# Kernel tuning notes

Hardware: AMD Instinct MI355X
Metric: run time of the kernel (lower is better)

The kernel has to match this reference:

```python
import jax, jax.numpy as jnp
import numpy as np

B, N, IN_DIM, OUT_DIM, H = 8, 1024, 512, 512, 8
SUP = OUT_DIM // H  # support_dim per head = 64


def setup_inputs() -> dict:
    key = jax.random.key(0)
    ks = jax.random.split(key, 6)
    # 0/1 dense adjacency with self-loops so no row is fully masked
    A = jax.random.randint(ks[0], (B, N, N), 0, 2).astype(jnp.float32)
    A = jnp.maximum(A, jnp.eye(N, dtype=jnp.float32)[None])
    X = jax.random.normal(ks[1], (B, N, IN_DIM), dtype=jnp.float32)
    # parameters, uniform(-1/sqrt(fan_last), 1/sqrt(fan_last)) as in reset_parameters
    sw = 1.0 / np.sqrt(SUP)
    W = jax.random.uniform(ks[2], (H, IN_DIM, SUP), minval=-sw, maxval=sw, dtype=jnp.float32)
    w1 = jax.random.uniform(ks[3], (H, SUP), minval=-sw, maxval=sw, dtype=jnp.float32)
    w2 = jax.random.uniform(ks[4], (H, SUP), minval=-sw, maxval=sw, dtype=jnp.float32)
    b = jax.random.uniform(ks[5], (2, H), minval=-1.0, maxval=1.0, dtype=jnp.float32)
    b1, b2 = b[0], b[1]
    return {"A": A, "X": X, "W": W, "w1": w1, "b1": b1, "w2": w2, "b2": b2}


def reference(A, X, W, w1, b1, w2, b2):
    # per-head projection: [B,H,N,SUP]
    inputs = jnp.einsum('bni,hio->bhno', X, W)
    # additive attention logits: self_fc [B,H,N,1] + neigh_fc [B,H,1,N]
    self_fc = jnp.einsum('bhno,ho->bhn', inputs, w1) + b1[None, :, None]
    neigh_fc = jnp.einsum('bhno,ho->bhn', inputs, w2) + b2[None, :, None]
    logits = jax.nn.leaky_relu(self_fc[..., :, None] + neigh_fc[..., None, :], 0.01)
    mask = -1e9 * (1.0 - A)  # [B,N,N]
    alphas = jax.nn.softmax(logits + mask[:, None], axis=-1)  # [B,H,N,N]
    out = jnp.einsum('bhnm,bhmo->bhno', alphas, inputs)
    out = jax.nn.relu(out)  # default activation = torch.relu
    # concat heads on last dim (head i contiguous), matching torch.cat
    return out.transpose(0, 2, 1, 3).reshape(B, N, H * SUP)
```

## Files before the change

kernel.cpp:

```cpp
#include <hip/hip_runtime.h>
#include <hip/hip_fp16.h>

#define BB 8
#define NN 1024
#define IN_DIM 512
#define HH 8
#define SUP 64
#define HS (HH * SUP)

typedef _Float16 half8 __attribute__((ext_vector_type(8)));
typedef float floatx4 __attribute__((ext_vector_type(4)));

__global__ __launch_bounds__(256) void k0_transpose_w(const float* __restrict__ W,
                                                      _Float16* __restrict__ Wt) {
    __shared__ float tile[64][65];
    const int it = blockIdx.x;
    const int h  = blockIdx.y;
    const int t  = threadIdx.x;
    {
        const int i  = t >> 2;
        const int o0 = (t & 3) * 16;
        const float* src = W + ((size_t)h * IN_DIM + it * 64 + i) * SUP + o0;
#pragma unroll
        for (int j = 0; j < 4; j++) {
            float4 v = ((const float4*)src)[j];
            tile[i][o0 + j * 4 + 0] = v.x;
            tile[i][o0 + j * 4 + 1] = v.y;
            tile[i][o0 + j * 4 + 2] = v.z;
            tile[i][o0 + j * 4 + 3] = v.w;
        }
    }
    __syncthreads();
    {
        const int o  = t >> 2;
        const int i0 = (t & 3) * 16;
        _Float16 buf[16];
#pragma unroll
        for (int j = 0; j < 16; j++) buf[j] = (_Float16)tile[i0 + j][o];
        _Float16* dst = Wt + ((size_t)h * SUP + o) * IN_DIM + it * 64 + i0;
        *(half8*)dst       = *(half8*)buf;
        *(half8*)(dst + 8) = *(half8*)(buf + 8);
    }
}

__global__ __launch_bounds__(256) void kpack(const float* __restrict__ A,
                                             unsigned char* __restrict__ Am) {
    const int gw   = blockIdx.x * 4 + (threadIdx.x >> 6);
    const int lane = threadIdx.x & 63;
    const float* arow = A + (size_t)gw * NN;
    unsigned long long keep = 0;
#pragma unroll
    for (int g = 0; g < 16; g++) {
        float a = arow[g * 64 + lane];
        unsigned long long bal = __ballot(a > 0.5f);
        if (lane == g) keep = bal;
    }
    if (lane < 16)
        *(unsigned long long*)(Am + (size_t)gw * 128 + lane * 8) = keep;
}

__global__ __launch_bounds__(256) void k1_proj(const float* __restrict__ X,
                                               const _Float16* __restrict__ Wt,
                                               const float* __restrict__ w1,
                                               const float* __restrict__ b1,
                                               const float* __restrict__ w2,
                                               const float* __restrict__ b2,
                                               _Float16* __restrict__ Pt,
                                               float* __restrict__ s_g,
                                               float* __restrict__ t_g,
                                               float* __restrict__ tmax16) {
    __shared__ __align__(16) _Float16 xs[64 * 40];
    __shared__ __align__(16) _Float16 wsh[64 * 40];
    __shared__ __align__(16) _Float16 po[64 * 72];
    __shared__ float tred[64];

    const int bh = blockIdx.y;
    const int b  = bh >> 3;
    const int h  = bh & 7;
    const int n0 = blockIdx.x * 64;
    const int t    = threadIdx.x;
    const int wave = t >> 6;
    const int lane = t & 63;
    const int quad = lane >> 4;
    const int l15  = lane & 15;
    const int row  = t >> 2;
    const int koff = (t & 3) * 8;

    floatx4 acc[4];
#pragma unroll
    for (int i = 0; i < 4; i++) acc[i] = {0.f, 0.f, 0.f, 0.f};

    float w1v[4], w2v[4];
#pragma unroll
    for (int ct = 0; ct < 4; ct++) {
        w1v[ct] = w1[h * 64 + ct * 16 + l15];
        w2v[ct] = w2[h * 64 + ct * 16 + l15];
    }
    const float b1h = b1[h];
    const float b2h = b2[h];

    const float*    xbase = X + ((size_t)b * NN + n0 + row) * IN_DIM;
    const _Float16* wbase = Wt + ((size_t)h * SUP + row) * IN_DIM;

    float4 xa = ((const float4*)(xbase + koff))[0];
    float4 xb = ((const float4*)(xbase + koff))[1];
    half8  wv = *(const half8*)(wbase + koff);

    for (int k0 = 0; k0 < IN_DIM; k0 += 32) {
        {
            _Float16 xh[8] = {(_Float16)xa.x, (_Float16)xa.y, (_Float16)xa.z, (_Float16)xa.w,
                              (_Float16)xb.x, (_Float16)xb.y, (_Float16)xb.z, (_Float16)xb.w};
            *(half8*)&xs[row * 40 + koff] = *(half8*)xh;
            *(half8*)&wsh[row * 40 + koff] = wv;
        }
        __syncthreads();
        if (k0 + 32 < IN_DIM) {
            const float* src = xbase + k0 + 32 + koff;
            xa = ((const float4*)src)[0];
            xb = ((const float4*)src)[1];
            wv = *(const half8*)(wbase + k0 + 32 + koff);
        }
        half8 af = *(const half8*)&xs[(wave * 16 + l15) * 40 + quad * 8];
#pragma unroll
        for (int ct = 0; ct < 4; ct++) {
            half8 bf = *(const half8*)&wsh[(ct * 16 + l15) * 40 + quad * 8];
            acc[ct] = __builtin_amdgcn_mfma_f32_16x16x32_f16(af, bf, acc[ct], 0, 0, 0);
        }
        __syncthreads();
    }

#pragma unroll
    for (int ct = 0; ct < 4; ct++) {
#pragma unroll
        for (int r = 0; r < 4; r++) {
            int o = ct * 16 + l15;
            int n = wave * 16 + quad * 4 + r;
            po[o * 72 + n] = (_Float16)acc[ct][r];
        }
    }
#pragma unroll
    for (int r = 0; r < 4; r++) {
        float sp = 0.f, tp = 0.f;
#pragma unroll
        for (int ct = 0; ct < 4; ct++) {
            sp += acc[ct][r] * w1v[ct];
            tp += acc[ct][r] * w2v[ct];
        }
#pragma unroll
        for (int off = 1; off < 16; off <<= 1) {
            sp += __shfl_xor(sp, off);
            tp += __shfl_xor(tp, off);
        }
        if (l15 == 0) {
            const int n = wave * 16 + quad * 4 + r;
            s_g[(size_t)bh * NN + n0 + n] = sp + b1h;
            float tv = tp + b2h;
            t_g[(size_t)bh * NN + n0 + n] = tv;
            tred[n] = tv;
        }
    }
    __syncthreads();
    {
        const int o   = t >> 2;
        const int nof = (t & 3) * 16;
        _Float16* dst = Pt + ((size_t)bh * SUP + o) * NN + n0 + nof;
        *(half8*)dst       = *(const half8*)&po[o * 72 + nof];
        *(half8*)(dst + 8) = *(const half8*)&po[o * 72 + nof + 8];
    }
    if (t == 0) {
        float m = -1e30f;
#pragma unroll
        for (int i = 0; i < 64; i++) m = fmaxf(m, tred[i]);
        tmax16[bh * 16 + blockIdx.x] = m;
    }
}

__global__ __launch_bounds__(256) void k2_attn(const unsigned char* __restrict__ Am,
                                               const _Float16* __restrict__ Pt,
                                               const float* __restrict__ s_g,
                                               const float* __restrict__ t_g,
                                               const float* __restrict__ tmax16,
                                               float* __restrict__ out) {
    __shared__ __align__(16) _Float16 vts[64 * 136];
    __shared__ __align__(16) float tl[NN];
    __shared__ __align__(16) unsigned char am[64 * 144];
    __shared__ float zinv_l[64];

    const int bh = blockIdx.y;
    const int b  = bh >> 3;
    const int h  = bh & 7;
    const int n0 = blockIdx.x * 64;
    const int t    = threadIdx.x;
    const int wave = t >> 6;
    const int lane = t & 63;
    const int quad = lane >> 4;
    const int l15  = lane & 15;
    const int row4 = t >> 2;
    const int seg  = t & 3;

    ((float4*)tl)[t] = ((const float4*)(t_g + (size_t)bh * NN))[t];
    {
        const uint4* asrc = (const uint4*)(Am + ((size_t)b * NN + n0 + row4) * 128 + seg * 32);
        uint4 ma = asrc[0], mb = asrc[1];
        *(uint4*)&am[row4 * 144 + seg * 32]      = ma;
        *(uint4*)&am[row4 * 144 + seg * 32 + 16] = mb;
    }
    float tmax = -1e30f;
#pragma unroll
    for (int i = 0; i < 16; i++) tmax = fmaxf(tmax, tmax16[bh * 16 + i]);

    const int myrow = wave * 16 + l15;
    const float sv = s_g[(size_t)bh * NN + n0 + myrow];
    const float xc = sv + tmax;
    const float cv = fmaxf(xc, 0.01f * xc);

    floatx4 acc[4];
#pragma unroll
    for (int i = 0; i < 4; i++) acc[i] = {0.f, 0.f, 0.f, 0.f};
    float zp = 0.f;

    const _Float16* pb = Pt + ((size_t)bh * SUP + row4) * NN + seg * 32;
    half8 v0 = ((const half8*)pb)[0];
    half8 v1 = ((const half8*)pb)[1];
    half8 v2 = ((const half8*)pb)[2];
    half8 v3 = ((const half8*)pb)[3];

    for (int mt = 0; mt < 8; mt++) {
        const int m0 = mt * 128;
        {
            _Float16* d = &vts[row4 * 136 + seg * 32];
            ((half8*)d)[0] = v0; ((half8*)d)[1] = v1;
            ((half8*)d)[2] = v2; ((half8*)d)[3] = v3;
        }
        __syncthreads();
        if (mt < 7) {
            const _Float16* p = pb + m0 + 128;
            v0 = ((const half8*)p)[0];
            v1 = ((const half8*)p)[1];
            v2 = ((const half8*)p)[2];
            v3 = ((const half8*)p)[3];
        }
#pragma unroll
        for (int kk = 0; kk < 4; kk++) {
            const unsigned mbyte = am[myrow * 144 + mt * 16 + kk * 4 + quad];
            const int kbase = m0 + kk * 32 + quad * 8;
            float4 ta = *(const float4*)&tl[kbase];
            float4 tb = *(const float4*)&tl[kbase + 4];
            float tv[8] = {ta.x, ta.y, ta.z, ta.w, tb.x, tb.y, tb.z, tb.w};
            _Float16 wb[8];
#pragma unroll
            for (int j = 0; j < 8; j++) {
                float x = sv + tv[j];
                float l = fmaxf(x, 0.01f * x);
                float e = __expf(l - cv);
                float we = (mbyte & (1u << j)) ? e : 0.f;
                zp += we;
                wb[j] = (_Float16)we;
            }
            half8 af = *(half8*)wb;
#pragma unroll
            for (int ct = 0; ct < 4; ct++) {
                half8 bf = *(const half8*)&vts[(ct * 16 + l15) * 136 + kk * 32 + quad * 8];
                acc[ct] = __builtin_amdgcn_mfma_f32_16x16x32_f16(af, bf, acc[ct], 0, 0, 0);
            }
        }
        __syncthreads();
    }

    zp += __shfl_xor(zp, 16);
    zp += __shfl_xor(zp, 32);
    if (quad == 0) zinv_l[myrow] = 1.0f / zp;
    __syncthreads();

#pragma unroll
    for (int r = 0; r < 4; r++) {
        const int rr = wave * 16 + quad * 4 + r;
        const float rz = zinv_l[rr];
#pragma unroll
        for (int ct = 0; ct < 4; ct++) {
            float v = acc[ct][r] * rz;
            v = v > 0.f ? v : 0.f;
            out[((size_t)b * NN + n0 + rr) * HS + h * SUP + ct * 16 + l15] = v;
        }
    }
}

extern "C" void kernel_launch(void* const* d_in, const int* in_sizes, int n_in,
                              void* d_out, int out_size, void* d_ws, size_t ws_size,
                              hipStream_t stream) {
    const float* A  = (const float*)d_in[0];
    const float* X  = (const float*)d_in[1];
    const float* W  = (const float*)d_in[2];
    const float* w1 = (const float*)d_in[3];
    const float* b1 = (const float*)d_in[4];
    const float* w2 = (const float*)d_in[5];
    const float* b2 = (const float*)d_in[6];
    float* out = (float*)d_out;

    char* ws = (char*)d_ws;
    _Float16*      Wt     = (_Float16*)(ws);
    _Float16*      Pt     = (_Float16*)(ws + 524288);
    float*         s_g    = (float*)(ws + 8912896);
    float*         t_g    = (float*)(ws + 9175040);
    float*         tmax16 = (float*)(ws + 9437184);
    unsigned char* Am     = (unsigned char*)(ws + 9441280);

    hipLaunchKernelGGL(k0_transpose_w, dim3(IN_DIM / 64, HH), dim3(256), 0, stream, W, Wt);
    hipLaunchKernelGGL(kpack, dim3(BB * NN / 4), dim3(256), 0, stream, A, Am);
    hipLaunchKernelGGL(k1_proj, dim3(NN / 64, BB * HH), dim3(256), 0, stream,
                       X, Wt, w1, b1, w2, b2, Pt, s_g, t_g, tmax16);
    hipLaunchKernelGGL(k2_attn, dim3(NN / 64, BB * HH), dim3(256), 0, stream,
                       Am, Pt, s_g, t_g, tmax16, out);
}
```

Measured before the change: 140.6 us.

## Merge prep kernels, double-buffer LDS tiles, widen attention blocks to 128 rows

Fuses the weight-transpose and adjacency-packing kernels into one launch to cut a kernel launch. Double-buffers the LDS tiles in both the projection and attention kernels so one barrier per iteration is removed. The attention kernel now handles 128 query rows per 512-thread block, reading mask words straight from global into registers and sharing the softmax normaliser through a wave shuffle instead of LDS. This halves the grid, raises per-block LDS use, and adds register pressure from the extra mask prefetch.

```diff
diff --git a/kernel.cpp b/kernel.cpp
--- a/kernel.cpp
+++ b/kernel.cpp
@@ -11,52 +11,55 @@
 typedef _Float16 half8 __attribute__((ext_vector_type(8)));
 typedef float floatx4 __attribute__((ext_vector_type(4)));
 
-__global__ __launch_bounds__(256) void k0_transpose_w(const float* __restrict__ W,
-                                                      _Float16* __restrict__ Wt) {
+__global__ __launch_bounds__(256) void kprep(const float* __restrict__ A,
+                                             unsigned char* __restrict__ Am,
+                                             const float* __restrict__ W,
+                                             _Float16* __restrict__ Wt) {
     __shared__ float tile[64][65];
-    const int it = blockIdx.x;
-    const int h  = blockIdx.y;
-    const int t  = threadIdx.x;
-    {
-        const int i  = t >> 2;
-        const int o0 = (t & 3) * 16;
-        const float* src = W + ((size_t)h * IN_DIM + it * 64 + i) * SUP + o0;
-#pragma unroll
-        for (int j = 0; j < 4; j++) {
-            float4 v = ((const float4*)src)[j];
-            tile[i][o0 + j * 4 + 0] = v.x;
-            tile[i][o0 + j * 4 + 1] = v.y;
-            tile[i][o0 + j * 4 + 2] = v.z;
-            tile[i][o0 + j * 4 + 3] = v.w;
-        }
-    }
-    __syncthreads();
-    {
-        const int o  = t >> 2;
-        const int i0 = (t & 3) * 16;
-        _Float16 buf[16];
-#pragma unroll
-        for (int j = 0; j < 16; j++) buf[j] = (_Float16)tile[i0 + j][o];
-        _Float16* dst = Wt + ((size_t)h * SUP + o) * IN_DIM + it * 64 + i0;
-        *(half8*)dst       = *(half8*)buf;
-        *(half8*)(dst + 8) = *(half8*)(buf + 8);
-    }
-}
-
-__global__ __launch_bounds__(256) void kpack(const float* __restrict__ A,
-                                             unsigned char* __restrict__ Am) {
-    const int gw   = blockIdx.x * 4 + (threadIdx.x >> 6);
-    const int lane = threadIdx.x & 63;
-    const float* arow = A + (size_t)gw * NN;
-    unsigned long long keep = 0;
-#pragma unroll
-    for (int g = 0; g < 16; g++) {
-        float a = arow[g * 64 + lane];
-        unsigned long long bal = __ballot(a > 0.5f);
-        if (lane == g) keep = bal;
-    }
-    if (lane < 16)
-        *(unsigned long long*)(Am + (size_t)gw * 128 + lane * 8) = keep;
+    const int bid = blockIdx.x;
+    const int t   = threadIdx.x;
+    if (bid < 2048) {
+        const int gw   = bid * 4 + (t >> 6);
+        const int lane = t & 63;
+        const float* arow = A + (size_t)gw * NN;
+        unsigned long long keep = 0;
+#pragma unroll
+        for (int g = 0; g < 16; g++) {
+            float a = arow[g * 64 + lane];
+            unsigned long long bal = __ballot(a > 0.5f);
+            if (lane == g) keep = bal;
+        }
+        if (lane < 16)
+            *(unsigned long long*)(Am + (size_t)gw * 128 + lane * 8) = keep;
+    } else {
+        const int wb = bid - 2048;
+        const int it = wb & 7;
+        const int h  = wb >> 3;
+        {
+            const int i  = t >> 2;
+            const int o0 = (t & 3) * 16;
+            const float* src = W + ((size_t)h * IN_DIM + it * 64 + i) * SUP + o0;
+#pragma unroll
+            for (int j = 0; j < 4; j++) {
+                float4 v = ((const float4*)src)[j];
+                tile[i][o0 + j * 4 + 0] = v.x;
+                tile[i][o0 + j * 4 + 1] = v.y;
+                tile[i][o0 + j * 4 + 2] = v.z;
+                tile[i][o0 + j * 4 + 3] = v.w;
+            }
+        }
+        __syncthreads();
+        {
+            const int o  = t >> 2;
+            const int i0 = (t & 3) * 16;
+            _Float16 buf[16];
+#pragma unroll
+            for (int j = 0; j < 16; j++) buf[j] = (_Float16)tile[i0 + j][o];
+            _Float16* dst = Wt + ((size_t)h * SUP + o) * IN_DIM + it * 64 + i0;
+            *(half8*)dst       = *(half8*)buf;
+            *(half8*)(dst + 8) = *(half8*)(buf + 8);
+        }
+    }
 }
 
 __global__ __launch_bounds__(256) void k1_proj(const float* __restrict__ X,
@@ -69,8 +72,8 @@
                                                float* __restrict__ s_g,
                                                float* __restrict__ t_g,
                                                float* __restrict__ tmax16) {
-    __shared__ __align__(16) _Float16 xs[64 * 40];
-    __shared__ __align__(16) _Float16 wsh[64 * 40];
+    __shared__ __align__(16) _Float16 xs[2][64 * 40];
+    __shared__ __align__(16) _Float16 wsh[2][64 * 40];
     __shared__ __align__(16) _Float16 po[64 * 72];
     __shared__ float tred[64];
 
@@ -106,28 +109,29 @@
     float4 xb = ((const float4*)(xbase + koff))[1];
     half8  wv = *(const half8*)(wbase + koff);
 
-    for (int k0 = 0; k0 < IN_DIM; k0 += 32) {
+    for (int it = 0; it < 16; it++) {
+        const int cur = it & 1;
         {
             _Float16 xh[8] = {(_Float16)xa.x, (_Float16)xa.y, (_Float16)xa.z, (_Float16)xa.w,
                               (_Float16)xb.x, (_Float16)xb.y, (_Float16)xb.z, (_Float16)xb.w};
-            *(half8*)&xs[row * 40 + koff] = *(half8*)xh;
-            *(half8*)&wsh[row * 40 + koff] = wv;
+            *(half8*)&xs[cur][row * 40 + koff]  = *(half8*)xh;
+            *(half8*)&wsh[cur][row * 40 + koff] = wv;
         }
         __syncthreads();
-        if (k0 + 32 < IN_DIM) {
-            const float* src = xbase + k0 + 32 + koff;
+        if (it < 15) {
+            const float* src = xbase + (it + 1) * 32 + koff;
             xa = ((const float4*)src)[0];
             xb = ((const float4*)src)[1];
-            wv = *(const half8*)(wbase + k0 + 32 + koff);
-        }
-        half8 af = *(const half8*)&xs[(wave * 16 + l15) * 40 + quad * 8];
+            wv = *(const half8*)(wbase + (it + 1) * 32 + koff);
+        }
+        half8 af = *(const half8*)&xs[cur][(wave * 16 + l15) * 40 + quad * 8];
 #pragma unroll
         for (int ct = 0; ct < 4; ct++) {
-            half8 bf = *(const half8*)&wsh[(ct * 16 + l15) * 40 + quad * 8];
+            half8 bf = *(const half8*)&wsh[cur][(ct * 16 + l15) * 40 + quad * 8];
             acc[ct] = __builtin_amdgcn_mfma_f32_16x16x32_f16(af, bf, acc[ct], 0, 0, 0);
         }
-        __syncthreads();
-    }
+    }
+    __syncthreads();
 
 #pragma unroll
     for (int ct = 0; ct < 4; ct++) {
@@ -175,36 +179,29 @@
     }
 }
 
-__global__ __launch_bounds__(256) void k2_attn(const unsigned char* __restrict__ Am,
+__global__ __launch_bounds__(512) void k2_attn(const unsigned char* __restrict__ Am,
                                                const _Float16* __restrict__ Pt,
                                                const float* __restrict__ s_g,
                                                const float* __restrict__ t_g,
                                                const float* __restrict__ tmax16,
                                                float* __restrict__ out) {
-    __shared__ __align__(16) _Float16 vts[64 * 136];
+    __shared__ __align__(16) _Float16 vts[2][64 * 136];
     __shared__ __align__(16) float tl[NN];
-    __shared__ __align__(16) unsigned char am[64 * 144];
-    __shared__ float zinv_l[64];
 
     const int bh = blockIdx.y;
     const int b  = bh >> 3;
     const int h  = bh & 7;
-    const int n0 = blockIdx.x * 64;
+    const int n0 = blockIdx.x * 128;
     const int t    = threadIdx.x;
     const int wave = t >> 6;
     const int lane = t & 63;
     const int quad = lane >> 4;
     const int l15  = lane & 15;
-    const int row4 = t >> 2;
-    const int seg  = t & 3;
-
-    ((float4*)tl)[t] = ((const float4*)(t_g + (size_t)bh * NN))[t];
-    {
-        const uint4* asrc = (const uint4*)(Am + ((size_t)b * NN + n0 + row4) * 128 + seg * 32);
-        uint4 ma = asrc[0], mb = asrc[1];
-        *(uint4*)&am[row4 * 144 + seg * 32]      = ma;
-        *(uint4*)&am[row4 * 144 + seg * 32 + 16] = mb;
-    }
+    const int row4 = t >> 3;
+    const int seg  = t & 7;
+
+    ((float2*)tl)[t] = ((const float2*)(t_g + (size_t)bh * NN))[t];
+
     float tmax = -1e30f;
 #pragma unroll
     for (int i = 0; i < 16; i++) tmax = fmaxf(tmax, tmax16[bh * 16 + i]);
@@ -219,30 +216,32 @@
     for (int i = 0; i < 4; i++) acc[i] = {0.f, 0.f, 0.f, 0.f};
     float zp = 0.f;
 
-    const _Float16* pb = Pt + ((size_t)bh * SUP + row4) * NN + seg * 32;
+    const _Float16* pb = Pt + ((size_t)bh * SUP + row4) * NN + seg * 16;
     half8 v0 = ((const half8*)pb)[0];
     half8 v1 = ((const half8*)pb)[1];
-    half8 v2 = ((const half8*)pb)[2];
-    half8 v3 = ((const half8*)pb)[3];
+    const uint4* mrow = (const uint4*)(Am + ((size_t)b * NN + n0 + myrow) * 128);
+    uint4 mcur = mrow[0];
 
     for (int mt = 0; mt < 8; mt++) {
-        const int m0 = mt * 128;
+        const int cur = mt & 1;
         {
-            _Float16* d = &vts[row4 * 136 + seg * 32];
-            ((half8*)d)[0] = v0; ((half8*)d)[1] = v1;
-            ((half8*)d)[2] = v2; ((half8*)d)[3] = v3;
+            _Float16* d = &vts[cur][row4 * 136 + seg * 16];
+            ((half8*)d)[0] = v0;
+            ((half8*)d)[1] = v1;
         }
         __syncthreads();
+        uint4 mnext;
         if (mt < 7) {
-            const _Float16* p = pb + m0 + 128;
+            const _Float16* p = pb + (mt + 1) * 128;
             v0 = ((const half8*)p)[0];
             v1 = ((const half8*)p)[1];
-            v2 = ((const half8*)p)[2];
-            v3 = ((const half8*)p)[3];
-        }
+            mnext = mrow[mt + 1];
+        }
+        const unsigned mw[4] = {mcur.x, mcur.y, mcur.z, mcur.w};
+        const int m0 = mt * 128;
 #pragma unroll
         for (int kk = 0; kk < 4; kk++) {
-            const unsigned mbyte = am[myrow * 144 + mt * 16 + kk * 4 + quad];
+            const unsigned mbyte = (mw[kk] >> (quad * 8)) & 0xffu;
             const int kbase = m0 + kk * 32 + quad * 8;
             float4 ta = *(const float4*)&tl[kbase];
             float4 tb = *(const float4*)&tl[kbase + 4];
@@ -260,22 +259,21 @@
             half8 af = *(half8*)wb;
 #pragma unroll
             for (int ct = 0; ct < 4; ct++) {
-                half8 bf = *(const half8*)&vts[(ct * 16 + l15) * 136 + kk * 32 + quad * 8];
+                half8 bf = *(const half8*)&vts[cur][(ct * 16 + l15) * 136 + kk * 32 + quad * 8];
                 acc[ct] = __builtin_amdgcn_mfma_f32_16x16x32_f16(af, bf, acc[ct], 0, 0, 0);
             }
         }
-        __syncthreads();
+        if (mt < 7) mcur = mnext;
     }
 
     zp += __shfl_xor(zp, 16);
     zp += __shfl_xor(zp, 32);
-    if (quad == 0) zinv_l[myrow] = 1.0f / zp;
-    __syncthreads();
+    const float rzown = 1.0f / zp;
 
 #pragma unroll
     for (int r = 0; r < 4; r++) {
         const int rr = wave * 16 + quad * 4 + r;
-        const float rz = zinv_l[rr];
+        const float rz = __shfl(rzown, quad * 20 + r);
 #pragma unroll
         for (int ct = 0; ct < 4; ct++) {
             float v = acc[ct][r] * rz;
@@ -305,10 +303,9 @@
     float*         tmax16 = (float*)(ws + 9437184);
     unsigned char* Am     = (unsigned char*)(ws + 9441280);
 
-    hipLaunchKernelGGL(k0_transpose_w, dim3(IN_DIM / 64, HH), dim3(256), 0, stream, W, Wt);
-    hipLaunchKernelGGL(kpack, dim3(BB * NN / 4), dim3(256), 0, stream, A, Am);
+    hipLaunchKernelGGL(kprep, dim3(2048 + 64), dim3(256), 0, stream, A, Am, W, Wt);
     hipLaunchKernelGGL(k1_proj, dim3(NN / 64, BB * HH), dim3(256), 0, stream,
                        X, Wt, w1, b1, w2, b2, Pt, s_g, t_g, tmax16);
-    hipLaunchKernelGGL(k2_attn, dim3(NN / 64, BB * HH), dim3(256), 0, stream,
+    hipLaunchKernelGGL(k2_attn, dim3(NN / 128, BB * HH), dim3(512), 0, stream,
                        Am, Pt, s_g, t_g, tmax16, out);
 }
```

Measured after the change: 136.7 us. -2.8%, faster.
